# Kernel tuning notes

Measured on AMD Instinct MI355X. Metric: run time of the kernel, lower is better.

## Reference

```python
import jax, jax.numpy as jnp
import numpy as np
import math

B, S, D, H = 2, 2048, 1024, 16
HD = D // H            # head dim = 64
E, K = 8, 2            # routed experts, top-k
HM = 1024              # moe_inter_dim (multiple_of=256 keeps it)
HS = 1024              # shared expert hidden = moe_inter_dim * n_shared_experts
EPS = 1e-6
TEMP = 1.0


def setup_inputs() -> dict:
    key = jax.random.key(0)
    ks = jax.random.split(key, 16)
    s = 0.02
    x = jax.random.normal(ks[0], (B, S, D), jnp.float32)
    # RoPE angles: theta = 10000
    inv_freq = 1.0 / (10000.0 ** (np.arange(0, HD, 2, dtype=np.float32) / HD))  # (HD//2,)
    ang = np.arange(S, dtype=np.float32)[:, None] * inv_freq[None, :]           # (S, HD//2)
    freqs_cos = jnp.asarray(np.cos(ang))
    freqs_sin = jnp.asarray(np.sin(ang))
    return {
        "x": x,
        "freqs_cos": freqs_cos,
        "freqs_sin": freqs_sin,
        "att_norm_w": jnp.ones((D,), jnp.float32),
        "ffn_norm_w": jnp.ones((D,), jnp.float32),
        "wq": jax.random.normal(ks[1], (D, D), jnp.float32) * s,
        "wk": jax.random.normal(ks[2], (D, D), jnp.float32) * s,
        "wv": jax.random.normal(ks[3], (D, D), jnp.float32) * s,
        "wo": jax.random.normal(ks[4], (D, D), jnp.float32) * s,
        "gate_w": jax.random.normal(ks[5], (E, D), jnp.float32) * s,
        "ew1": jax.random.normal(ks[6], (E, D, HM), jnp.float32) * s,
        "ew2": jax.random.normal(ks[7], (E, HM, D), jnp.float32) * s,
        "ew3": jax.random.normal(ks[8], (E, D, HM), jnp.float32) * s,
        "sw1": jax.random.normal(ks[9], (D, HS), jnp.float32) * s,
        "sw2": jax.random.normal(ks[10], (HS, D), jnp.float32) * s,
        "sw3": jax.random.normal(ks[11], (D, HS), jnp.float32) * s,
    }


def _rmsnorm(x, w):
    return x * jax.lax.rsqrt(jnp.mean(x * x, axis=-1, keepdims=True) + EPS) * w


def _rope(t, cos, sin):
    # t: (B,H,S,HD); rotate pairs (even, odd) like complex multiply
    tr = t.reshape(B, H, S, HD // 2, 2)
    t0, t1 = tr[..., 0], tr[..., 1]
    c = cos[None, None, :, :]
    s_ = sin[None, None, :, :]
    o0 = t0 * c - t1 * s_
    o1 = t0 * s_ + t1 * c
    return jnp.stack([o0, o1], axis=-1).reshape(B, H, S, HD)


def reference(x, freqs_cos, freqs_sin, att_norm_w, ffn_norm_w,
              wq, wk, wv, wo, gate_w, ew1, ew2, ew3, sw1, sw2, sw3):
    # ---- attention sub-block ----
    xn = _rmsnorm(x, att_norm_w)
    q = (xn @ wq).reshape(B, S, H, HD).transpose(0, 2, 1, 3)  # (B,H,S,HD)
    k = (xn @ wk).reshape(B, S, H, HD).transpose(0, 2, 1, 3)
    v = (xn @ wv).reshape(B, S, H, HD).transpose(0, 2, 1, 3)
    q = _rope(q, freqs_cos, freqs_sin)
    k = _rope(k, freqs_cos, freqs_sin)
    scores = jnp.einsum('bhqd,bhkd->bhqk', q, k) / math.sqrt(HD)
    attn = jax.nn.softmax(scores, axis=-1)
    out = jnp.einsum('bhqk,bhkd->bhqd', attn, v)
    out = out.transpose(0, 2, 1, 3).reshape(B, S, D) @ wo
    h = x + out

    # ---- MoE sub-block ----
    xf = _rmsnorm(h, ffn_norm_w).reshape(-1, D)  # (N,D), N=B*S
    # shared expert (SwiGLU)
    shared = (jax.nn.silu(xf @ sw1) * (xf @ sw3)) @ sw2
    # gate (eval mode: no noise)
    g_scores = (xf @ gate_w.T) / TEMP
    probs = jax.nn.softmax(g_scores, axis=-1)          # (N,E)
    vals, idx = jax.lax.top_k(probs, K)                 # (N,K)
    vals = vals / (jnp.sum(vals, axis=-1, keepdims=True) + 1e-9)
    # per-token per-expert weight (equivalent to scatter into expert_mask)
    mask = jnp.sum(jax.nn.one_hot(idx, E, dtype=xf.dtype) * vals[..., None], axis=1)  # (N,E)
    # routed experts: dense per-expert SwiGLU, weighted combine (zero weight => no contribution)
    h1 = jax.nn.silu(jnp.einsum('nd,edh->enh', xf, ew1)) * jnp.einsum('nd,edh->enh', xf, ew3)
    eo = jnp.einsum('enh,ehd->end', h1, ew2)            # (E,N,D)
    y = jnp.einsum('end,ne->nd', eo, mask) + shared
    return h + y.reshape(B, S, D)
```

## Files before the change

kernel.cpp:

```cpp
#include <hip/hip_runtime.h>
#include <hip/hip_bf16.h>
#include <stdint.h>


typedef __hip_bfloat16 bf16;
typedef __attribute__((ext_vector_type(8))) __bf16 bf16x8;
typedef __attribute__((ext_vector_type(4))) float f32x4;
typedef __attribute__((ext_vector_type(16))) float f32x16;
typedef __attribute__((ext_vector_type(2))) unsigned int u32x2;

#define S_  2048
#define D_  1024
#define N_  4096

__device__ __forceinline__ float b2f(bf16 h) { return __bfloat162float(h); }
__device__ __forceinline__ bf16  f2b(float f) { return __float2bfloat16(f); }

__device__ __forceinline__ bf16x8 ld_bf16x8(const bf16* p) {
    union { uint4 u; bf16x8 v; } x;
    x.u = *(const uint4*)p;
    return x.v;
}

__device__ __forceinline__ void gload_lds16(const void* gsrc, void* ldst) {
    __builtin_amdgcn_global_load_lds(
        (__attribute__((address_space(1))) void*)const_cast<void*>(gsrc),
        (__attribute__((address_space(3))) void*)ldst, 16, 0, 0);
}

__device__ __forceinline__ u32x2 tr16_read(unsigned lds_off) {
    u32x2 d;
    asm volatile("ds_read_b64_tr_b16 %0, %1" : "=v"(d) : "v"(lds_off));
    return d;
}

__device__ __forceinline__ int swz4(int r) { return ((r >> 1) ^ (r >> 3)) & 3; }

__global__ __launch_bounds__(256)
void transpose_all(const float* __restrict__ wq, const float* __restrict__ wk,
                   const float* __restrict__ wv, const float* __restrict__ wo,
                   const float* __restrict__ ew1, const float* __restrict__ ew2,
                   const float* __restrict__ ew3, const float* __restrict__ sw1,
                   const float* __restrict__ sw2, const float* __restrict__ sw3,
                   bf16* __restrict__ wqkv_t, bf16* __restrict__ wo_t,
                   bf16* __restrict__ ew13_t, bf16* __restrict__ ew2_t)
{
    __shared__ float t[64][65];
    const int z = blockIdx.z;
    const float* in; bf16* out; int rm = 1, ro = 0;
    if (z < 3)        { in = (z == 0 ? wq : z == 1 ? wk : wv); out = wqkv_t + (size_t)z * 1048576; }
    else if (z == 3)  { in = wo; out = wo_t; }
    else if (z < 12)  { const int e = z - 4;  in = ew1 + (size_t)e * 1048576; out = ew13_t + (size_t)e * 2097152; rm = 2; ro = 0; }
    else if (z < 20)  { const int e = z - 12; in = ew3 + (size_t)e * 1048576; out = ew13_t + (size_t)e * 2097152; rm = 2; ro = 1; }
    else if (z < 28)  { const int e = z - 20; in = ew2 + (size_t)e * 1048576; out = ew2_t + (size_t)e * 1048576; }
    else if (z == 28) { in = sw1; out = ew13_t + (size_t)8 * 2097152; rm = 2; ro = 0; }
    else if (z == 29) { in = sw3; out = ew13_t + (size_t)8 * 2097152; rm = 2; ro = 1; }
    else              { in = sw2; out = ew2_t + (size_t)8 * 1048576; }

    const int c0 = blockIdx.x * 64, r0 = blockIdx.y * 64;
    const int tx = (threadIdx.x & 15) * 4, ty = threadIdx.x >> 4;
#pragma unroll
    for (int i = 0; i < 4; i++)
        *(float4*)&t[ty + i * 16][tx] = *(const float4*)(in + (size_t)(r0 + ty + i * 16) * 1024 + c0 + tx);
    __syncthreads();
#pragma unroll
    for (int i = 0; i < 4; i++) {
        const int lc = ty + i * 16;
        union { bf16 h[4]; uint2 u; } pk;
#pragma unroll
        for (int j = 0; j < 4; j++) pk.h[j] = f2b(t[tx + j][lc]);
        *(uint2*)&out[(size_t)((c0 + lc) * rm + ro) * 1024 + r0 + tx] = pk.u;
    }
}

__global__ __launch_bounds__(256)
void rmsnorm_kernel(const float* __restrict__ x, const float* __restrict__ w,
                    bf16* __restrict__ out)
{
    const int n = blockIdx.x;
    const int tid = threadIdx.x;
    const float4 v = *(const float4*)(x + (size_t)n * D_ + tid * 4);
    float ss = v.x * v.x + v.y * v.y + v.z * v.z + v.w * v.w;
#pragma unroll
    for (int m = 1; m < 64; m <<= 1) ss += __shfl_xor(ss, m);
    __shared__ float red[4];
    if ((tid & 63) == 0) red[tid >> 6] = ss;
    __syncthreads();
    const float tot = red[0] + red[1] + red[2] + red[3];
    const float rstd = rsqrtf(tot * (1.0f / D_) + 1e-6f);
    const float4 wv = *(const float4*)(w + tid * 4);
    union { bf16 h[4]; uint2 u; } pk;
    pk.h[0] = f2b(v.x * rstd * wv.x);
    pk.h[1] = f2b(v.y * rstd * wv.y);
    pk.h[2] = f2b(v.z * rstd * wv.z);
    pk.h[3] = f2b(v.w * rstd * wv.w);
    *(uint2*)(out + (size_t)n * D_ + tid * 4) = pk.u;
}

template<int EPI, int MODE>
__global__ __launch_bounds__(512)
void gemm_bt(const bf16* __restrict__ A, const bf16* __restrict__ Bt,
             void* __restrict__ Cout, const float* __restrict__ resid,
             int M, int Kdim, int lda, int ldb, int ldc, long bstride,
             const int* __restrict__ tlist, const int* __restrict__ offs,
             const float* __restrict__ fc, const float* __restrict__ fs)
{
    __shared__ bf16 As[2][128 * 32];
    __shared__ bf16 Bs[2][128 * 32];
    const int tid = threadIdx.x;
    const int wave = tid >> 6, lane = tid & 63;

    int bx, by;
    if constexpr (MODE == 0) {
        const int gx = gridDim.x;
        const int nwg = gx * gridDim.y;
        int flat = blockIdx.y * gx + blockIdx.x;
        flat = (flat & 7) * (nwg >> 3) + (flat >> 3);
        bx = flat % gx; by = flat / gx;
    } else {
        bx = blockIdx.x; by = blockIdx.y;
    }

    int mcount = M, outBase = 0;
    const bf16* Bp = Bt;
    if (MODE != 0) {
        const int e = blockIdx.z;
        outBase = offs[e];
        mcount = offs[e + 1] - outBase;
        Bp = Bt + (size_t)e * bstride;
    }
    const int m0 = by * 128;
    if (m0 >= mcount) return;
    const int n0 = bx * 128;

    const int srow = tid >> 2;
    const int sc4 = tid & 3;
    const int scol = (sc4 ^ swz4(srow)) * 8;
    int rA = m0 + srow;
    if (rA >= mcount) rA = mcount - 1;
    long arow;
    if (MODE == 1)      arow = tlist[outBase + rA];
    else if (MODE == 2) arow = (long)outBase + rA;
    else                arow = rA;
    const bf16* aptr = A + (size_t)arow * lda + scol;
    const bf16* bptr = Bp + (size_t)(n0 + srow) * ldb + scol;

    f32x16 acc[2];
#pragma unroll
    for (int tm = 0; tm < 2; tm++)
#pragma unroll
        for (int i = 0; i < 16; i++) acc[tm][i] = 0.f;

    const int wm = (wave >> 2) * 64, wn = (wave & 3) * 32;
    const int l31 = lane & 31, l5 = lane >> 5;

    int aoff[2][2], boff[2];
#pragma unroll
    for (int tm = 0; tm < 2; tm++) {
        const int ra = wm + tm * 32 + l31;
#pragma unroll
        for (int kk = 0; kk < 2; kk++)
            aoff[tm][kk] = ra * 32 + ((kk * 2 + l5) ^ swz4(ra)) * 8;
    }
    {
        const int rb = wn + l31;
#pragma unroll
        for (int kk = 0; kk < 2; kk++)
            boff[kk] = rb * 32 + ((kk * 2 + l5) ^ swz4(rb)) * 8;
    }

    const int nkt = Kdim >> 5;
    gload_lds16(aptr, (char*)&As[0][0] + wave * 1024);
    gload_lds16(bptr, (char*)&Bs[0][0] + wave * 1024);

    int p = 0;
    for (int kt = 0; kt < nkt; kt++) {
        if (kt + 1 < nkt) {
            const int ko = (kt + 1) << 5;
            gload_lds16(aptr + ko, (char*)&As[p ^ 1][0] + wave * 1024);
            gload_lds16(bptr + ko, (char*)&Bs[p ^ 1][0] + wave * 1024);
            asm volatile("s_waitcnt vmcnt(2)" ::: "memory");
        } else {
            asm volatile("s_waitcnt vmcnt(0)" ::: "memory");
        }
        asm volatile("s_barrier" ::: "memory");

        const bf16* Ab = &As[p][0];
        const bf16* Bb = &Bs[p][0];
#pragma unroll
        for (int kk = 0; kk < 2; kk++) {
            const bf16x8 bf0 = ld_bf16x8(&Bb[boff[kk]]);
            const bf16x8 af0 = ld_bf16x8(&Ab[aoff[0][kk]]);
            const bf16x8 af1 = ld_bf16x8(&Ab[aoff[1][kk]]);
            acc[0] = __builtin_amdgcn_mfma_f32_32x32x16_bf16(af0, bf0, acc[0], 0, 0, 0);
            acc[1] = __builtin_amdgcn_mfma_f32_32x32x16_bf16(af1, bf0, acc[1], 0, 0, 0);
        }

        asm volatile("s_barrier" ::: "memory");
        p ^= 1;
    }

#pragma unroll
    for (int tm = 0; tm < 2; tm++)
#pragma unroll
        for (int i = 0; i < 16; i++) {
            const int r = m0 + wm + tm * 32 + (i & 3) + 8 * (i >> 2) + 4 * l5;
            const int c = n0 + wn + l31;
            const float v = acc[tm][i];
            if (EPI == 3) {
                const float other = __shfl_xor(v, 1);
                const float res = (v / (1.f + __expf(-v))) * other;
                if (((lane & 1) == 0) && r < mcount)
                    ((bf16*)Cout)[(size_t)(outBase + r) * ldc + (c >> 1)] = f2b(res);
            } else if (EPI == 4) {
                const float other = __shfl_xor(v, 1);
                float o = v;
                if (c < 2048) {
                    const int s = r & (S_ - 1);
                    const int jf = (c & 63) >> 1;
                    const float co = fc[s * 32 + jf], si = fs[s * 32 + jf];
                    o = v * co + other * ((c & 1) ? si : -si);
                    if (c < 1024) o *= 0.125f;
                }
                ((bf16*)Cout)[(size_t)r * ldc + c] = f2b(o);
            } else if (r < mcount) {
                const size_t oi = (size_t)(outBase + r) * ldc + c;
                if (EPI == 0)      ((bf16*)Cout)[oi] = f2b(v);
                else if (EPI == 1) ((float*)Cout)[oi] = v;
                else               ((float*)Cout)[oi] = resid[oi] + v;
            }
        }
}

__global__ __launch_bounds__(256)
void attn_kernel(const bf16* __restrict__ qkv, bf16* __restrict__ out)
{
    __shared__ __align__(16) bf16 Ks[64 * 72];
    __shared__ __align__(16) bf16 Vs[4 * 1032 + 8];
    const int tid = threadIdx.x, wave = tid >> 6, lane = tid & 63;
    const int b = blockIdx.z, hh = blockIdx.y;
    const int q0 = blockIdx.x * 128;
    const bf16* base  = qkv + ((size_t)b * S_) * 3072 + (size_t)hh * 64;
    const bf16* kbase = base + 1024;
    const bf16* vbase = base + 2048;
    const int fr = lane & 15, fg = lane >> 4;

    bf16x8 aq[2][2];
#pragma unroll
    for (int qb = 0; qb < 2; qb++)
#pragma unroll
        for (int s2 = 0; s2 < 2; s2++)
            aq[qb][s2] = ld_bf16x8(base + (size_t)(q0 + wave * 32 + qb * 16 + fr) * 3072 + s2 * 32 + fg * 8);

    f32x4 zero4 = {0.f, 0.f, 0.f, 0.f};
    f32x4 acc_o[2][4];
    float mrow[2], lrow[2];
#pragma unroll
    for (int qb = 0; qb < 2; qb++) {
#pragma unroll
        for (int hf = 0; hf < 4; hf++) acc_o[qb][hf] = zero4;
        mrow[qb] = -1e30f; lrow[qb] = 0.f;
    }

    const int srow = tid >> 2, sc4 = tid & 3;
    const unsigned vtr0 =
        (unsigned)(uintptr_t)(__attribute__((address_space(3))) void*)&Vs[0] + lane * 8;

    uint4 kg0, kg1, vg0, vg1;
    {
        const bf16* kr = kbase + (size_t)srow * 3072 + sc4 * 16;
        kg0 = *(const uint4*)kr; kg1 = *(const uint4*)(kr + 8);
        const bf16* vr = vbase + (size_t)srow * 3072 + sc4 * 16;
        vg0 = *(const uint4*)vr; vg1 = *(const uint4*)(vr + 8);
    }

    for (int kv0 = 0; kv0 < S_; kv0 += 64) {
        __syncthreads();
        *(uint4*)&Ks[srow * 72 + sc4 * 16]         = kg0;
        *(uint4*)&Ks[srow * 72 + sc4 * 16 + 8]     = kg1;
        *(uint4*)&Vs[sc4 * 1032 + srow * 16]       = vg0;
        *(uint4*)&Vs[sc4 * 1032 + srow * 16 + 8]   = vg1;
        __syncthreads();
        if (kv0 + 64 < S_) {
            const bf16* kr = kbase + (size_t)(kv0 + 64 + srow) * 3072 + sc4 * 16;
            kg0 = *(const uint4*)kr; kg1 = *(const uint4*)(kr + 8);
            const bf16* vr = vbase + (size_t)(kv0 + 64 + srow) * 3072 + sc4 * 16;
            vg0 = *(const uint4*)vr; vg1 = *(const uint4*)(vr + 8);
        }

        f32x4 sc[4][2];
#pragma unroll
        for (int kt = 0; kt < 4; kt++)
#pragma unroll
            for (int qb = 0; qb < 2; qb++) sc[kt][qb] = zero4;
        __builtin_amdgcn_s_setprio(1);
#pragma unroll
        for (int kt = 0; kt < 4; kt++) {
            const bf16x8 k0 = ld_bf16x8(&Ks[(kt * 16 + fr) * 72 + fg * 8]);
            const bf16x8 k1 = ld_bf16x8(&Ks[(kt * 16 + fr) * 72 + 32 + fg * 8]);
#pragma unroll
            for (int qb = 0; qb < 2; qb++) {
                sc[kt][qb] = __builtin_amdgcn_mfma_f32_16x16x32_bf16(k0, aq[qb][0], sc[kt][qb], 0, 0, 0);
                sc[kt][qb] = __builtin_amdgcn_mfma_f32_16x16x32_bf16(k1, aq[qb][1], sc[kt][qb], 0, 0, 0);
            }
        }
        __builtin_amdgcn_s_setprio(0);

        bf16x8 pcomb[2][2];
        float scalv[2];
#pragma unroll
        for (int qb = 0; qb < 2; qb++) {
            float pm = -1e30f;
#pragma unroll
            for (int kt = 0; kt < 4; kt++)
#pragma unroll
                for (int j = 0; j < 4; j++) pm = fmaxf(pm, sc[kt][qb][j]);
            pm = fmaxf(pm, __shfl_xor(pm, 16));
            pm = fmaxf(pm, __shfl_xor(pm, 32));
            const float mnew = fmaxf(mrow[qb], pm);
            const float scal = __expf(mrow[qb] - mnew);
            mrow[qb] = mnew;
            float ps = 0.f;
            union { bf16 h[16]; bf16x8 v8[2]; } pk;
#pragma unroll
            for (int kt = 0; kt < 4; kt++)
#pragma unroll
                for (int j = 0; j < 4; j++) {
                    const float p = __expf(sc[kt][qb][j] - mnew);
                    ps += p;
                    pk.h[kt * 4 + j] = f2b(p);
                }
            pcomb[qb][0] = pk.v8[0];
            pcomb[qb][1] = pk.v8[1];
            ps += __shfl_xor(ps, 16);
            ps += __shfl_xor(ps, 32);
            lrow[qb] = lrow[qb] * scal + ps;
            scalv[qb] = scal;
        }

#pragma unroll
        for (int j = 0; j < 4; j++) {
            const int src = (lane & 48) + fg * 4 + j;
            const float s0 = __shfl(scalv[0], src);
            const float s1 = __shfl(scalv[1], src);
#pragma unroll
            for (int hf = 0; hf < 4; hf++) {
                acc_o[0][hf][j] *= s0;
                acc_o[1][hf][j] *= s1;
            }
        }

#pragma unroll
        for (int tp = 0; tp < 2; tp++) {
            union { u32x2 d2[2]; bf16x8 v8; } vc[4];
#pragma unroll
            for (int hf = 0; hf < 4; hf++) {
                vc[hf].d2[0] = tr16_read(vtr0 + hf * 2064 + (tp * 2)     * 512);
                vc[hf].d2[1] = tr16_read(vtr0 + hf * 2064 + (tp * 2 + 1) * 512);
            }
            asm volatile("s_waitcnt lgkmcnt(0)" ::: "memory");
            __builtin_amdgcn_sched_barrier(0);
            __builtin_amdgcn_s_setprio(1);
#pragma unroll
            for (int hf = 0; hf < 4; hf++)
#pragma unroll
                for (int qb = 0; qb < 2; qb++)
                    acc_o[qb][hf] = __builtin_amdgcn_mfma_f32_16x16x32_bf16(
                        pcomb[qb][tp], vc[hf].v8, acc_o[qb][hf], 0, 0, 0);
            __builtin_amdgcn_s_setprio(0);
        }
    }

#pragma unroll
    for (int qb = 0; qb < 2; qb++) {
        const float inv = 1.f / lrow[qb];
#pragma unroll
        for (int j = 0; j < 4; j++) {
            const float ij = __shfl(inv, (lane & 48) + fg * 4 + j);
            const int r = q0 + wave * 32 + qb * 16 + fg * 4 + j;
#pragma unroll
            for (int hf = 0; hf < 4; hf++)
                out[((size_t)(b * S_ + r)) * D_ + hh * 64 + hf * 16 + fr] =
                    f2b(acc_o[qb][hf][j] * ij);
        }
    }
}

__global__ __launch_bounds__(256)
void gating_kernel(const float* __restrict__ h, const float* __restrict__ gw,
                   const float* __restrict__ wnorm,
                   int* __restrict__ top_idx, float* __restrict__ top_w)
{
    const int wave = threadIdx.x >> 6, lane = threadIdx.x & 63;
    const int n = blockIdx.x * 4 + wave;
    const float* hr = h + (size_t)n * D_;
    float acc[8] = {0.f, 0.f, 0.f, 0.f, 0.f, 0.f, 0.f, 0.f};
    float ss = 0.f;
    for (int d = lane * 4; d < D_; d += 256) {
        const float4 hv = *(const float4*)(hr + d);
        const float4 wv = *(const float4*)(wnorm + d);
        ss += hv.x * hv.x + hv.y * hv.y + hv.z * hv.z + hv.w * hv.w;
        const float x0 = hv.x * wv.x, x1 = hv.y * wv.y, x2 = hv.z * wv.z, x3 = hv.w * wv.w;
#pragma unroll
        for (int e2 = 0; e2 < 8; e2++) {
            const float4 gv = *(const float4*)(gw + e2 * D_ + d);
            acc[e2] += x0 * gv.x + x1 * gv.y + x2 * gv.z + x3 * gv.w;
        }
    }
#pragma unroll
    for (int m = 1; m < 64; m <<= 1) {
        ss += __shfl_xor(ss, m);
#pragma unroll
        for (int e2 = 0; e2 < 8; e2++) acc[e2] += __shfl_xor(acc[e2], m);
    }
    if (lane == 0) {
        const float rstd = rsqrtf(ss * (1.0f / D_) + 1e-6f);
        float s[8];
#pragma unroll
        for (int e2 = 0; e2 < 8; e2++) s[e2] = acc[e2] * rstd;
        int e0 = 0;
#pragma unroll
        for (int e2 = 1; e2 < 8; e2++) if (s[e2] > s[e0]) e0 = e2;
        int e1 = (e0 == 0) ? 1 : 0;
#pragma unroll
        for (int e2 = 0; e2 < 8; e2++) if (e2 != e0 && s[e2] > s[e1]) e1 = e2;
        const float mx = s[e0];
        float Z = 0.f;
        float p[8];
#pragma unroll
        for (int e2 = 0; e2 < 8; e2++) { p[e2] = __expf(s[e2] - mx); Z += p[e2]; }
        const float v0 = p[e0] / Z, v1 = p[e1] / Z;
        const float sm = v0 + v1 + 1e-9f;
        top_idx[n * 2] = e0; top_idx[n * 2 + 1] = e1;
        top_w[n * 2] = v0 / sm; top_w[n * 2 + 1] = v1 / sm;
    }
}

__global__ __launch_bounds__(1024)
void route_kernel(const int* __restrict__ top_idx, int* __restrict__ offs,
                  int* __restrict__ token_list, int* __restrict__ tok_pos)
{
    __shared__ int hist[8];
    __shared__ int base[8];
    const int tid = threadIdx.x;
    if (tid < 8) hist[tid] = 0;
    __syncthreads();
    int4 e4a = *(const int4*)(top_idx + tid * 8);
    int4 e4b = *(const int4*)(top_idx + tid * 8 + 4);
    int myidx[8] = {e4a.x, e4a.y, e4a.z, e4a.w, e4b.x, e4b.y, e4b.z, e4b.w};
#pragma unroll
    for (int i = 0; i < 8; i++) atomicAdd(&hist[myidx[i]], 1);
    __syncthreads();
    if (tid == 0) {
        int o = 0;
#pragma unroll
        for (int e = 0; e < 8; e++) { base[e] = o; offs[e] = o; o += hist[e]; }
        offs[8] = o;
        offs[9] = o + N_;
    }
    __syncthreads();
    if (tid < 8) hist[tid] = 0;
    __syncthreads();
#pragma unroll
    for (int i = 0; i < 8; i++) {
        const int entry = tid * 8 + i;
        const int e = myidx[i];
        const int pos = base[e] + atomicAdd(&hist[e], 1);
        token_list[pos] = entry >> 1;
        tok_pos[entry] = pos;
    }
#pragma unroll
    for (int i = 0; i < 4; i++)
        token_list[2 * N_ + tid * 4 + i] = tid * 4 + i;
}

__global__ __launch_bounds__(256)
void combine_kernel(const float* __restrict__ h, const bf16* __restrict__ eo,
                    const int* __restrict__ tok_pos, const float* __restrict__ top_w,
                    float* __restrict__ out)
{
    const int idx = blockIdx.x * 256 + threadIdx.x;
    const int n = idx >> 8;
    const int c = (idx & 255) * 4;
    const float4 hv = *(const float4*)(h + (size_t)n * D_ + c);
    const int p0 = tok_pos[n * 2], p1 = tok_pos[n * 2 + 1];
    const float w0 = top_w[n * 2], w1 = top_w[n * 2 + 1];
    union { uint2 u; bf16 hh[4]; } a0, a1, ash;
    a0.u  = *(const uint2*)(eo + (size_t)p0 * D_ + c);
    a1.u  = *(const uint2*)(eo + (size_t)p1 * D_ + c);
    ash.u = *(const uint2*)(eo + (size_t)(2 * N_ + n) * D_ + c);
    float4 r;
    r.x = hv.x + b2f(ash.hh[0]) + w0 * b2f(a0.hh[0]) + w1 * b2f(a1.hh[0]);
    r.y = hv.y + b2f(ash.hh[1]) + w0 * b2f(a0.hh[1]) + w1 * b2f(a1.hh[1]);
    r.z = hv.z + b2f(ash.hh[2]) + w0 * b2f(a0.hh[2]) + w1 * b2f(a1.hh[2]);
    r.w = hv.w + b2f(ash.hh[3]) + w0 * b2f(a0.hh[3]) + w1 * b2f(a1.hh[3]);
    *(float4*)(out + (size_t)n * D_ + c) = r;
}

extern "C" void kernel_launch(void* const* d_in, const int* in_sizes, int n_in,
                              void* d_out, int out_size, void* d_ws, size_t ws_size,
                              hipStream_t stream)
{
    const float* x   = (const float*)d_in[0];
    const float* fc  = (const float*)d_in[1];
    const float* fs  = (const float*)d_in[2];
    const float* anw = (const float*)d_in[3];
    const float* fnw = (const float*)d_in[4];
    const float* wq  = (const float*)d_in[5];
    const float* wk  = (const float*)d_in[6];
    const float* wv  = (const float*)d_in[7];
    const float* wo  = (const float*)d_in[8];
    const float* gw  = (const float*)d_in[9];
    const float* ew1 = (const float*)d_in[10];
    const float* ew2 = (const float*)d_in[11];
    const float* ew3 = (const float*)d_in[12];
    const float* sw1 = (const float*)d_in[13];
    const float* sw2 = (const float*)d_in[14];
    const float* sw3 = (const float*)d_in[15];

    char* ws = (char*)d_ws;
    bf16*  wqkv_t = (bf16*)(ws + 0);
    bf16*  wo_t   = (bf16*)(ws + 6291456);
    bf16*  ew13_t = (bf16*)(ws + 8388608);
    bf16*  ew2_t  = (bf16*)(ws + 46137344);
    bf16*  xn     = (bf16*)(ws + 65011712);
    bf16*  qkv    = (bf16*)(ws + 73400320);
    bf16*  attn   = (bf16*)(ws + 98566144);
    float* hbuf   = (float*)(ws + 106954752);
    bf16*  eo     = (bf16*)(ws + 123731968);
    char*  misc   = ws + 148897792;
    int*   offs       = (int*)(misc + 0);
    int*   top_idx    = (int*)(misc + 128);
    float* top_w      = (float*)(misc + 128 + 32768);
    int*   token_list = (int*)(misc + 128 + 65536);
    int*   tok_pos    = (int*)(misc + 128 + 131072);

    const dim3 tb(256);
    const dim3 tb512(512);
    transpose_all<<<dim3(16, 16, 31), tb, 0, stream>>>(
        wq, wk, wv, wo, ew1, ew2, ew3, sw1, sw2, sw3,
        wqkv_t, wo_t, ew13_t, ew2_t);

    rmsnorm_kernel<<<N_, tb, 0, stream>>>(x, anw, xn);
    gemm_bt<4, 0><<<dim3(24, 32, 1), tb512, 0, stream>>>(xn, wqkv_t, qkv, nullptr,
        N_, 1024, 1024, 1024, 3072, 0, nullptr, nullptr, fc, fs);
    attn_kernel<<<dim3(16, 16, 2), tb, 0, stream>>>(qkv, attn);
    gemm_bt<2, 0><<<dim3(8, 32, 1), tb512, 0, stream>>>(attn, wo_t, hbuf, x,
        N_, 1024, 1024, 1024, 1024, 0, nullptr, nullptr, nullptr, nullptr);

    rmsnorm_kernel<<<N_, tb, 0, stream>>>(hbuf, fnw, xn);
    gating_kernel<<<N_ / 4, tb, 0, stream>>>(hbuf, gw, fnw, top_idx, top_w);
    route_kernel<<<1, 1024, 0, stream>>>(top_idx, offs, token_list, tok_pos);

    gemm_bt<3, 1><<<dim3(16, 32, 9), tb512, 0, stream>>>(xn, ew13_t, qkv, nullptr,
        0, 1024, 1024, 1024, 1024, 2097152, token_list, offs, nullptr, nullptr);
    gemm_bt<0, 2><<<dim3(8, 32, 9), tb512, 0, stream>>>((const bf16*)qkv, ew2_t, eo, nullptr,
        0, 1024, 1024, 1024, 1024, 1048576, nullptr, offs, nullptr, nullptr);

    combine_kernel<<<4096, tb, 0, stream>>>(hbuf, eo, tok_pos, top_w, (float*)d_out);
}
```

Before: 353.7 us.

## Enlarge GEMM block tile to 256x128 with 64x64 per-wave tiles

Doubles the M dimension of the GEMM block tile and gives each wave a 64x64 output sub-tile with four MFMA accumulators, halving grid rows for all four GEMM launches. This raises MFMA work per LDS fragment load and halves B-tile global traffic per output. It increases accumulator registers and LDS use and reduces the number of workgroups, which can underfill the GPU for smaller GEMMs and the per-expert MoE GEMMs.

```diff
diff --git a/kernel.cpp b/kernel.cpp
--- a/kernel.cpp
+++ b/kernel.cpp
@@ -105,7 +105,7 @@
              const int* __restrict__ tlist, const int* __restrict__ offs,
              const float* __restrict__ fc, const float* __restrict__ fs)
 {
-    __shared__ bf16 As[2][128 * 32];
+    __shared__ bf16 As[2][256 * 32];
     __shared__ bf16 Bs[2][128 * 32];
     const int tid = threadIdx.x;
     const int wave = tid >> 6, lane = tid & 63;
@@ -129,57 +129,63 @@
         mcount = offs[e + 1] - outBase;
         Bp = Bt + (size_t)e * bstride;
     }
-    const int m0 = by * 128;
+    const int m0 = by * 256;
     if (m0 >= mcount) return;
     const int n0 = bx * 128;
 
     const int srow = tid >> 2;
     const int sc4 = tid & 3;
     const int scol = (sc4 ^ swz4(srow)) * 8;
-    int rA = m0 + srow;
-    if (rA >= mcount) rA = mcount - 1;
-    long arow;
-    if (MODE == 1)      arow = tlist[outBase + rA];
-    else if (MODE == 2) arow = (long)outBase + rA;
-    else                arow = rA;
-    const bf16* aptr = A + (size_t)arow * lda + scol;
+    const bf16* aptr[2];
+#pragma unroll
+    for (int j = 0; j < 2; j++) {
+        int rA = m0 + j * 128 + srow;
+        if (rA >= mcount) rA = mcount - 1;
+        long arow;
+        if (MODE == 1)      arow = tlist[outBase + rA];
+        else if (MODE == 2) arow = (long)outBase + rA;
+        else                arow = rA;
+        aptr[j] = A + (size_t)arow * lda + scol;
+    }
     const bf16* bptr = Bp + (size_t)(n0 + srow) * ldb + scol;
 
-    f32x16 acc[2];
+    f32x16 acc[2][2];
 #pragma unroll
     for (int tm = 0; tm < 2; tm++)
 #pragma unroll
-        for (int i = 0; i < 16; i++) acc[tm][i] = 0.f;
-
-    const int wm = (wave >> 2) * 64, wn = (wave & 3) * 32;
+        for (int tn = 0; tn < 2; tn++)
+#pragma unroll
+            for (int i = 0; i < 16; i++) acc[tm][tn][i] = 0.f;
+
+    const int wm = (wave >> 1) * 64, wn = (wave & 1) * 64;
     const int l31 = lane & 31, l5 = lane >> 5;
 
-    int aoff[2][2], boff[2];
+    int aoff[2][2], boff[2][2];
 #pragma unroll
     for (int tm = 0; tm < 2; tm++) {
         const int ra = wm + tm * 32 + l31;
-#pragma unroll
-        for (int kk = 0; kk < 2; kk++)
-            aoff[tm][kk] = ra * 32 + ((kk * 2 + l5) ^ swz4(ra)) * 8;
-    }
-    {
-        const int rb = wn + l31;
-#pragma unroll
-        for (int kk = 0; kk < 2; kk++)
-            boff[kk] = rb * 32 + ((kk * 2 + l5) ^ swz4(rb)) * 8;
+        const int rb = wn + tm * 32 + l31;
+#pragma unroll
+        for (int kk = 0; kk < 2; kk++) {
+            const int g = kk * 2 + l5;
+            aoff[tm][kk] = ra * 32 + (g ^ swz4(ra)) * 8;
+            boff[tm][kk] = rb * 32 + (g ^ swz4(rb)) * 8;
+        }
     }
 
     const int nkt = Kdim >> 5;
-    gload_lds16(aptr, (char*)&As[0][0] + wave * 1024);
-    gload_lds16(bptr, (char*)&Bs[0][0] + wave * 1024);
+    gload_lds16(aptr[0], (char*)&As[0][0] + wave * 1024);
+    gload_lds16(aptr[1], (char*)&As[0][0] + 8192 + wave * 1024);
+    gload_lds16(bptr,    (char*)&Bs[0][0] + wave * 1024);
 
     int p = 0;
     for (int kt = 0; kt < nkt; kt++) {
         if (kt + 1 < nkt) {
             const int ko = (kt + 1) << 5;
-            gload_lds16(aptr + ko, (char*)&As[p ^ 1][0] + wave * 1024);
-            gload_lds16(bptr + ko, (char*)&Bs[p ^ 1][0] + wave * 1024);
-            asm volatile("s_waitcnt vmcnt(2)" ::: "memory");
+            gload_lds16(aptr[0] + ko, (char*)&As[p ^ 1][0] + wave * 1024);
+            gload_lds16(aptr[1] + ko, (char*)&As[p ^ 1][0] + 8192 + wave * 1024);
+            gload_lds16(bptr + ko,    (char*)&Bs[p ^ 1][0] + wave * 1024);
+            asm volatile("s_waitcnt vmcnt(3)" ::: "memory");
         } else {
             asm volatile("s_waitcnt vmcnt(0)" ::: "memory");
         }
@@ -189,11 +195,14 @@
         const bf16* Bb = &Bs[p][0];
 #pragma unroll
         for (int kk = 0; kk < 2; kk++) {
-            const bf16x8 bf0 = ld_bf16x8(&Bb[boff[kk]]);
             const bf16x8 af0 = ld_bf16x8(&Ab[aoff[0][kk]]);
             const bf16x8 af1 = ld_bf16x8(&Ab[aoff[1][kk]]);
-            acc[0] = __builtin_amdgcn_mfma_f32_32x32x16_bf16(af0, bf0, acc[0], 0, 0, 0);
-            acc[1] = __builtin_amdgcn_mfma_f32_32x32x16_bf16(af1, bf0, acc[1], 0, 0, 0);
+            const bf16x8 bf0 = ld_bf16x8(&Bb[boff[0][kk]]);
+            const bf16x8 bf1 = ld_bf16x8(&Bb[boff[1][kk]]);
+            acc[0][0] = __builtin_amdgcn_mfma_f32_32x32x16_bf16(af0, bf0, acc[0][0], 0, 0, 0);
+            acc[0][1] = __builtin_amdgcn_mfma_f32_32x32x16_bf16(af0, bf1, acc[0][1], 0, 0, 0);
+            acc[1][0] = __builtin_amdgcn_mfma_f32_32x32x16_bf16(af1, bf0, acc[1][0], 0, 0, 0);
+            acc[1][1] = __builtin_amdgcn_mfma_f32_32x32x16_bf16(af1, bf1, acc[1][1], 0, 0, 0);
         }
 
         asm volatile("s_barrier" ::: "memory");
@@ -203,33 +212,35 @@
 #pragma unroll
     for (int tm = 0; tm < 2; tm++)
 #pragma unroll
-        for (int i = 0; i < 16; i++) {
-            const int r = m0 + wm + tm * 32 + (i & 3) + 8 * (i >> 2) + 4 * l5;
-            const int c = n0 + wn + l31;
-            const float v = acc[tm][i];
-            if (EPI == 3) {
-                const float other = __shfl_xor(v, 1);
-                const float res = (v / (1.f + __expf(-v))) * other;
-                if (((lane & 1) == 0) && r < mcount)
-                    ((bf16*)Cout)[(size_t)(outBase + r) * ldc + (c >> 1)] = f2b(res);
-            } else if (EPI == 4) {
-                const float other = __shfl_xor(v, 1);
-                float o = v;
-                if (c < 2048) {
-                    const int s = r & (S_ - 1);
-                    const int jf = (c & 63) >> 1;
-                    const float co = fc[s * 32 + jf], si = fs[s * 32 + jf];
-                    o = v * co + other * ((c & 1) ? si : -si);
-                    if (c < 1024) o *= 0.125f;
+        for (int tn = 0; tn < 2; tn++)
+#pragma unroll
+            for (int i = 0; i < 16; i++) {
+                const int r = m0 + wm + tm * 32 + (i & 3) + 8 * (i >> 2) + 4 * l5;
+                const int c = n0 + wn + tn * 32 + l31;
+                const float v = acc[tm][tn][i];
+                if (EPI == 3) {
+                    const float other = __shfl_xor(v, 1);
+                    const float res = (v / (1.f + __expf(-v))) * other;
+                    if (((lane & 1) == 0) && r < mcount)
+                        ((bf16*)Cout)[(size_t)(outBase + r) * ldc + (c >> 1)] = f2b(res);
+                } else if (EPI == 4) {
+                    const float other = __shfl_xor(v, 1);
+                    float o = v;
+                    if (c < 2048) {
+                        const int s = r & (S_ - 1);
+                        const int jf = (c & 63) >> 1;
+                        const float co = fc[s * 32 + jf], si = fs[s * 32 + jf];
+                        o = v * co + other * ((c & 1) ? si : -si);
+                        if (c < 1024) o *= 0.125f;
+                    }
+                    ((bf16*)Cout)[(size_t)r * ldc + c] = f2b(o);
+                } else if (r < mcount) {
+                    const size_t oi = (size_t)(outBase + r) * ldc + c;
+                    if (EPI == 0)      ((bf16*)Cout)[oi] = f2b(v);
+                    else if (EPI == 1) ((float*)Cout)[oi] = v;
+                    else               ((float*)Cout)[oi] = resid[oi] + v;
                 }
-                ((bf16*)Cout)[(size_t)r * ldc + c] = f2b(o);
-            } else if (r < mcount) {
-                const size_t oi = (size_t)(outBase + r) * ldc + c;
-                if (EPI == 0)      ((bf16*)Cout)[oi] = f2b(v);
-                else if (EPI == 1) ((float*)Cout)[oi] = v;
-                else               ((float*)Cout)[oi] = resid[oi] + v;
             }
-        }
 }
 
 __global__ __launch_bounds__(256)
@@ -542,19 +553,19 @@
         wqkv_t, wo_t, ew13_t, ew2_t);
 
     rmsnorm_kernel<<<N_, tb, 0, stream>>>(x, anw, xn);
-    gemm_bt<4, 0><<<dim3(24, 32, 1), tb512, 0, stream>>>(xn, wqkv_t, qkv, nullptr,
+    gemm_bt<4, 0><<<dim3(24, 16, 1), tb512, 0, stream>>>(xn, wqkv_t, qkv, nullptr,
         N_, 1024, 1024, 1024, 3072, 0, nullptr, nullptr, fc, fs);
     attn_kernel<<<dim3(16, 16, 2), tb, 0, stream>>>(qkv, attn);
-    gemm_bt<2, 0><<<dim3(8, 32, 1), tb512, 0, stream>>>(attn, wo_t, hbuf, x,
+    gemm_bt<2, 0><<<dim3(8, 16, 1), tb512, 0, stream>>>(attn, wo_t, hbuf, x,
         N_, 1024, 1024, 1024, 1024, 0, nullptr, nullptr, nullptr, nullptr);
 
     rmsnorm_kernel<<<N_, tb, 0, stream>>>(hbuf, fnw, xn);
     gating_kernel<<<N_ / 4, tb, 0, stream>>>(hbuf, gw, fnw, top_idx, top_w);
     route_kernel<<<1, 1024, 0, stream>>>(top_idx, offs, token_list, tok_pos);
 
-    gemm_bt<3, 1><<<dim3(16, 32, 9), tb512, 0, stream>>>(xn, ew13_t, qkv, nullptr,
+    gemm_bt<3, 1><<<dim3(16, 16, 9), tb512, 0, stream>>>(xn, ew13_t, qkv, nullptr,
         0, 1024, 1024, 1024, 1024, 2097152, token_list, offs, nullptr, nullptr);
-    gemm_bt<0, 2><<<dim3(8, 32, 9), tb512, 0, stream>>>((const bf16*)qkv, ew2_t, eo, nullptr,
+    gemm_bt<0, 2><<<dim3(8, 16, 9), tb512, 0, stream>>>((const bf16*)qkv, ew2_t, eo, nullptr,
         0, 1024, 1024, 1024, 1024, 1048576, nullptr, offs, nullptr, nullptr);
 
     combine_kernel<<<4096, tb, 0, stream>>>(hbuf, eo, tok_pos, top_w, (float*)d_out);
```

New measurement: 363.3 us. 2.7% more time.
